# Kernel tuning notes

Hardware: AMD Instinct MI355X
Metric: run time of the kernel (lower is better)

## Reference

```python
import jax, jax.numpy as jnp
import numpy as np

N_NODES = 100000
N_EDGES = 3200000  # avg degree 32
D_IN = 256
D_OUT = 256


def setup_inputs() -> dict:
    key = jax.random.key(0)
    k1, k2, k3, k4 = jax.random.split(key, 4)
    x = jax.random.normal(k1, (N_NODES, D_IN), dtype=jnp.float32)
    # nn.Linear(in, out, bias=False): weight shape [out, in]
    W = jax.random.normal(k2, (D_OUT, D_IN), dtype=jnp.float32) / np.sqrt(D_IN).astype(np.float32)
    bias = jnp.zeros((D_OUT,), dtype=jnp.float32)
    rows = jax.random.randint(k3, (N_EDGES,), 0, N_NODES, dtype=jnp.int32)
    cols = jax.random.randint(k4, (N_EDGES,), 0, N_NODES, dtype=jnp.int32)
    return {"x": x, "W": W, "bias": bias, "rows": rows, "cols": cols}


def reference(x, W, bias, rows, cols):
    # aggr == 'planetoid-gcn-residual' branch; dropout p=0 (identity).
    n = x.shape[0]
    h = x @ W.T + bias                                      # [N, D_out]
    # adj_t.sum(dim=-1): per-row degree of binary adjacency
    deg = jax.ops.segment_sum(jnp.ones(rows.shape, x.dtype), rows, num_segments=n)
    norm = jax.lax.rsqrt(1.0 + deg)[:, None]                # [N, 1]
    h = norm * h
    # spmm_add(adj_t, h)[i] = sum_{(i,j) in E} h[j]
    agg = jax.ops.segment_sum(h[cols], rows, num_segments=n)
    h = agg + h
    return norm * h
```

## Files before the change

kernel.cpp:

```cpp
#include <hip/hip_runtime.h>
#include <hip/hip_fp16.h>
#include <stdint.h>


#define THREADS 256
#define NB 512
#define B3_EDGES 8192

typedef _Float16 half8 __attribute__((ext_vector_type(8)));
typedef float floatx4 __attribute__((ext_vector_type(4)));

__global__ __launch_bounds__(THREADS) void bucket_count(
    const int* __restrict__ rows, int* __restrict__ bcnt, int E, int nbuck) {
    __shared__ int h[NB];
    h[threadIdx.x] = 0; h[threadIdx.x + 256] = 0;
    __syncthreads();
    int nquad  = E >> 2;
    int stride = gridDim.x * THREADS;
    for (int q = blockIdx.x * THREADS + threadIdx.x; q < nquad; q += stride) {
        int4 r = ((const int4*)rows)[q];
        atomicAdd(&h[r.x >> 8], 1);
        atomicAdd(&h[r.y >> 8], 1);
        atomicAdd(&h[r.z >> 8], 1);
        atomicAdd(&h[r.w >> 8], 1);
    }
    if (blockIdx.x == 0)
        for (int e = (nquad << 2) + threadIdx.x; e < E; e += THREADS)
            atomicAdd(&h[rows[e] >> 8], 1);
    __syncthreads();
    for (int b = threadIdx.x; b < nbuck; b += THREADS) {
        int v = h[b];
        if (v) atomicAdd(&bcnt[b], v);
    }
}

__global__ __launch_bounds__(THREADS) void bucket_scan(
    const int* __restrict__ bcnt, int* __restrict__ boff, int* __restrict__ bcur,
    int nbuck, int E) {
    __shared__ int s1[THREADS];
    int tid = threadIdx.x;
    int b0 = 2 * tid, b1 = 2 * tid + 1;
    int v0 = (b0 < nbuck) ? bcnt[b0] : 0;
    int v1 = (b1 < nbuck) ? bcnt[b1] : 0;
    s1[tid] = v0 + v1;
    __syncthreads();
    for (int off = 1; off < THREADS; off <<= 1) {
        int t = (tid >= off) ? s1[tid - off] : 0;
        __syncthreads();
        s1[tid] += t;
        __syncthreads();
    }
    int excl = s1[tid] - (v0 + v1);
    if (b0 < nbuck) { boff[b0] = excl;      bcur[b0] = excl; }
    if (b1 < nbuck) { boff[b1] = excl + v0; bcur[b1] = excl + v0; }
    if (tid == 0) boff[nbuck] = E;
}

__global__ __launch_bounds__(THREADS) void bucket_scatter(
    const int* __restrict__ rows, const int* __restrict__ cols,
    int* __restrict__ bcur, uint32_t* __restrict__ buf, int E, int nbuck) {
    __shared__ uint32_t staged[B3_EDGES];
    __shared__ int h[NB], lo[NB], gb[NB], hc[NB], s1[THREADS];
    int tid = threadIdx.x;
    h[tid] = 0; h[tid + 256] = 0;
    __syncthreads();
    int e0 = blockIdx.x * B3_EDGES;
    int e1 = e0 + B3_EDGES; if (e1 > E) e1 = E;
    for (int e = e0 + tid; e < e1; e += THREADS)
        atomicAdd(&h[rows[e] >> 8], 1);
    __syncthreads();
    int a0 = h[2 * tid], a1 = h[2 * tid + 1];
    s1[tid] = a0 + a1;
    __syncthreads();
    for (int off = 1; off < THREADS; off <<= 1) {
        int t = (tid >= off) ? s1[tid - off] : 0;
        __syncthreads();
        s1[tid] += t;
        __syncthreads();
    }
    int eps = s1[tid] - (a0 + a1);
    lo[2 * tid]     = eps;
    lo[2 * tid + 1] = eps + a0;
    for (int b = tid; b < NB; b += THREADS) {
        int v = h[b];
        gb[b] = (b < nbuck && v) ? atomicAdd(&bcur[b], v) : 0;
        hc[b] = 0;
    }
    __syncthreads();
    for (int e = e0 + tid; e < e1; e += THREADS) {
        int r = rows[e];
        int c = cols[e];
        int b = r >> 8;
        int p = lo[b] + atomicAdd(&hc[b], 1);
        staged[p] = ((uint32_t)(r & 255) << 17) | (uint32_t)c;
    }
    __syncthreads();
    int wid = tid >> 6, lane = tid & 63;
    for (int b = wid; b < nbuck; b += 4) {
        int cnt = h[b], src = lo[b], dst = gb[b];
        for (int i = lane; i < cnt; i += 64)
            buf[dst + i] = staged[src + i];
    }
}

__global__ __launch_bounds__(THREADS) void csr_finalize(
    const uint32_t* __restrict__ buf, const int* __restrict__ boff,
    int* __restrict__ rs, int* __restrict__ csr, int n, int E) {
    int b   = blockIdx.x;
    int tid = threadIdx.x;
    __shared__ int h[256], base[256], s1[THREADS];
    h[tid] = 0;
    __syncthreads();
    int s = boff[b], e = boff[b + 1];
    for (int i = s + tid; i < e; i += THREADS)
        atomicAdd(&h[buf[i] >> 17], 1);
    __syncthreads();
    int v = h[tid];
    s1[tid] = v;
    __syncthreads();
    for (int off = 1; off < THREADS; off <<= 1) {
        int t = (tid >= off) ? s1[tid - off] : 0;
        __syncthreads();
        s1[tid] += t;
        __syncthreads();
    }
    int myBase = s + s1[tid] - v;
    base[tid] = myBase;
    int row = (b << 8) + tid;
    if (row < n) rs[row] = myBase;
    h[tid] = 0;
    if (b == 0 && tid == 0) rs[n] = E;
    __syncthreads();
    for (int i = s + tid; i < e; i += THREADS) {
        uint32_t p = buf[i];
        int rl = p >> 17;
        int c  = p & 0x1FFFF;
        int q  = base[rl] + atomicAdd(&h[rl], 1);
        csr[q] = c;
    }
}

__global__ void make_bswz(const float* __restrict__ W, half8* __restrict__ Bswz) {
    int t = blockIdx.x * THREADS + threadIdx.x;
    int n_tile = t >> 9;
    int k_step = (t >> 6) & 7;
    int lane   = t & 63;
    int q = lane >> 4, m16 = lane & 15;
    const float* src = W + (size_t)(n_tile * 16 + m16) * 256 + k_step * 32 + q * 8;
    half8 h;
#pragma unroll
    for (int j = 0; j < 8; j++) h[j] = (_Float16)src[j];
    Bswz[t] = h;
}

__device__ __forceinline__ int As_swz(int b) {
    return b ^ ((((b >> 10) & 7) ^ (((b >> 8) & 1) << 3)) << 4);
}

__global__ __launch_bounds__(THREADS) void gemm_mfma(
    const float* __restrict__ x, const half8* __restrict__ Bswz,
    const float* __restrict__ bias, const int* __restrict__ rs,
    _Float16* __restrict__ h16, int n) {
    __shared__ _Float16 As[4 * 8 * 64 * 8];
    int tid  = threadIdx.x;
    int row0 = blockIdx.x * 64;

#pragma unroll
    for (int i = 0; i < 16; i++) {
        int flat = i * THREADS + tid;
        int r  = flat >> 6;
        int k  = (flat & 63) * 4;
        float4 v;
        if (row0 + r < n) v = *(const float4*)(x + (size_t)(row0 + r) * 256 + k);
        else { v.x = 0.f; v.y = 0.f; v.z = 0.f; v.w = 0.f; }
        int m_sub  = r >> 4;
        int k_step = k >> 5;
        int q      = (k >> 3) & 3;
        int j      = k & 7;
        int lane_w = (r & 15) + (q << 4);
        int entry  = (m_sub * 8 + k_step) * 64 + lane_w;
        union { _Float16 h[4]; uint2 u; } pk;
        pk.h[0] = (_Float16)v.x; pk.h[1] = (_Float16)v.y;
        pk.h[2] = (_Float16)v.z; pk.h[3] = (_Float16)v.w;
        *(uint2*)((char*)As + As_swz(entry * 16 + (j << 1))) = pk.u;
    }
    __syncthreads();

    int w    = tid >> 6;
    int lane = tid & 63;

    floatx4 acc[4][4];
#pragma unroll
    for (int ms = 0; ms < 4; ms++)
#pragma unroll
        for (int nn = 0; nn < 4; nn++) {
            acc[ms][nn][0] = 0.f; acc[ms][nn][1] = 0.f;
            acc[ms][nn][2] = 0.f; acc[ms][nn][3] = 0.f;
        }

    for (int ks = 0; ks < 8; ks++) {
        half8 bfrag[4];
#pragma unroll
        for (int nn = 0; nn < 4; nn++)
            bfrag[nn] = Bswz[((w * 4 + nn) * 8 + ks) * 64 + lane];
        half8 afrag[4];
#pragma unroll
        for (int ms = 0; ms < 4; ms++)
            afrag[ms] = *(const half8*)((char*)As +
                            As_swz(((ms * 8 + ks) * 64 + lane) * 16));
#pragma unroll
        for (int ms = 0; ms < 4; ms++)
#pragma unroll
            for (int nn = 0; nn < 4; nn++)
                acc[ms][nn] = __builtin_amdgcn_mfma_f32_16x16x32_f16(
                    afrag[ms], bfrag[nn], acc[ms][nn], 0, 0, 0);
    }

    int rgrp = lane >> 4;
    int cl   = lane & 15;
#pragma unroll
    for (int ms = 0; ms < 4; ms++) {
        int rbase = row0 + ms * 16 + rgrp * 4;
        float nrm[4];
#pragma unroll
        for (int i = 0; i < 4; i++) {
            int r = rbase + i;
            nrm[i] = (r < n) ? rsqrtf(1.0f + (float)(rs[r + 1] - rs[r])) : 0.f;
        }
#pragma unroll
        for (int nn = 0; nn < 4; nn++) {
            int col = w * 64 + nn * 16 + cl;
            float bb = bias[col];
#pragma unroll
            for (int i = 0; i < 4; i++) {
                int r = rbase + i;
                if (r < n)
                    h16[(size_t)r * 256 + col] =
                        (_Float16)((acc[ms][nn][i] + bb) * nrm[i]);
            }
        }
    }
}

__global__ __launch_bounds__(THREADS) void agg_rows(
    const _Float16* __restrict__ h16, const int* __restrict__ csr_col,
    const int* __restrict__ rs, float* __restrict__ out, int r0, int r1) {
    int row = r0 + blockIdx.x * 4 + (threadIdx.x >> 6);
    if (row >= r1) return;
    int lane = threadIdx.x & 63;
    int half = lane >> 5;
    int l32  = lane & 31;
    int off  = l32 * 8;

    int s   = rs[row];
    int end = rs[row + 1];

    float acc[8] = {0.f, 0.f, 0.f, 0.f, 0.f, 0.f, 0.f, 0.f};
    if (half == 0) {
        half8 v = *(const half8*)(h16 + (size_t)row * 256 + off);
#pragma unroll
        for (int j = 0; j < 8; j++) acc[j] = (float)v[j];
    }

    int e = s + half;
    for (; e + 2 < end; e += 4) {
        int c0 = csr_col[e];
        int c1 = csr_col[e + 2];
        half8 v0 = *(const half8*)(h16 + (size_t)c0 * 256 + off);
        half8 v1 = *(const half8*)(h16 + (size_t)c1 * 256 + off);
#pragma unroll
        for (int j = 0; j < 8; j++) acc[j] += (float)v0[j] + (float)v1[j];
    }
    for (; e < end; e += 2) {
        int c = csr_col[e];
        half8 v = *(const half8*)(h16 + (size_t)c * 256 + off);
#pragma unroll
        for (int j = 0; j < 8; j++) acc[j] += (float)v[j];
    }

#pragma unroll
    for (int j = 0; j < 8; j++) acc[j] += __shfl_down(acc[j], 32);

    if (half == 0) {
        float nrm = rsqrtf(1.0f + (float)(end - s));
        floatx4 o0, o1;
        o0[0] = acc[0] * nrm; o0[1] = acc[1] * nrm; o0[2] = acc[2] * nrm; o0[3] = acc[3] * nrm;
        o1[0] = acc[4] * nrm; o1[1] = acc[5] * nrm; o1[2] = acc[6] * nrm; o1[3] = acc[7] * nrm;
        float* dst = out + (size_t)row * 256 + off;
        __builtin_nontemporal_store(o0, (floatx4*)dst);
        __builtin_nontemporal_store(o1, (floatx4*)(dst + 4));
    }
}

extern "C" void kernel_launch(void* const* d_in, const int* in_sizes, int n_in,
                              void* d_out, int out_size, void* d_ws, size_t ws_size,
                              hipStream_t stream) {
    const float* x    = (const float*)d_in[0];
    const float* W    = (const float*)d_in[1];
    const float* bias = (const float*)d_in[2];
    const int*   rows = (const int*)d_in[3];
    const int*   cols = (const int*)d_in[4];

    const int D = 256;
    int n = in_sizes[0] / D;
    int E = in_sizes[3];
    int nbuck = (n + 255) >> 8;

    char* p = (char*)d_ws;
    auto alignup = [](size_t v) { return (v + 255) & ~(size_t)255; };
    _Float16* h16 = (_Float16*)p; p += alignup((size_t)n * D * sizeof(_Float16));
    int*   rs     = (int*)p;    p += alignup((size_t)(n + 1) * sizeof(int));
    int*   csr    = (int*)p;    p += alignup((size_t)E * sizeof(int));
    half8* Bswz   = (half8*)p;  p += alignup((size_t)8192 * sizeof(half8));
    int*   bcnt   = (int*)p;    p += alignup((size_t)NB * sizeof(int));
    int*   boff   = (int*)p;    p += alignup((size_t)(NB + 1) * sizeof(int));
    int*   bcur   = (int*)p;    p += alignup((size_t)NB * sizeof(int));

    uint32_t* buf = (uint32_t*)h16;

    hipMemsetAsync(bcnt, 0, (size_t)nbuck * sizeof(int), stream);

    bucket_count<<<256, THREADS, 0, stream>>>(rows, bcnt, E, nbuck);
    bucket_scan<<<1, THREADS, 0, stream>>>(bcnt, boff, bcur, nbuck, E);

    int b3blocks = (E + B3_EDGES - 1) / B3_EDGES;
    bucket_scatter<<<b3blocks, THREADS, 0, stream>>>(rows, cols, bcur, buf, E, nbuck);

    csr_finalize<<<nbuck, THREADS, 0, stream>>>(buf, boff, rs, csr, n, E);

    make_bswz<<<32, THREADS, 0, stream>>>(W, Bswz);

    int gblocks = (n + 63) / 64;
    gemm_mfma<<<gblocks, THREADS, 0, stream>>>(x, Bswz, bias, rs, h16, n);

    int chunk = (n + 7) / 8;
    for (int d = 0; d < 8; ++d) {
        int a0 = d * chunk;
        int a1 = a0 + chunk; if (a1 > n) a1 = n;
        if (a0 >= a1) break;
        int ablocks = (a1 - a0 + 3) / 4;
        agg_rows<<<ablocks, THREADS, 0, stream>>>(h16, csr, rs, (float*)d_out, a0, a1);
    }
}
```

Before: 595.8 us.

## Simplify GEMM A staging, double-buffer MFMA fragments, launch aggregation as two halves

After: 548.2 us. -8.0%, faster.

```diff
diff --git a/kernel.cpp b/kernel.cpp
--- a/kernel.cpp
+++ b/kernel.cpp
@@ -153,10 +153,6 @@
     Bswz[t] = h;
 }
 
-__device__ __forceinline__ int As_swz(int b) {
-    return b ^ ((((b >> 10) & 7) ^ (((b >> 8) & 1) << 3)) << 4);
-}
-
 __global__ __launch_bounds__(THREADS) void gemm_mfma(
     const float* __restrict__ x, const half8* __restrict__ Bswz,
     const float* __restrict__ bias, const int* __restrict__ rs,
@@ -166,23 +162,28 @@
     int row0 = blockIdx.x * 64;
 
 #pragma unroll
-    for (int i = 0; i < 16; i++) {
-        int flat = i * THREADS + tid;
-        int r  = flat >> 6;
-        int k  = (flat & 63) * 4;
-        float4 v;
-        if (row0 + r < n) v = *(const float4*)(x + (size_t)(row0 + r) * 256 + k);
-        else { v.x = 0.f; v.y = 0.f; v.z = 0.f; v.w = 0.f; }
-        int m_sub  = r >> 4;
-        int k_step = k >> 5;
-        int q      = (k >> 3) & 3;
-        int j      = k & 7;
-        int lane_w = (r & 15) + (q << 4);
-        int entry  = (m_sub * 8 + k_step) * 64 + lane_w;
-        union { _Float16 h[4]; uint2 u; } pk;
-        pk.h[0] = (_Float16)v.x; pk.h[1] = (_Float16)v.y;
-        pk.h[2] = (_Float16)v.z; pk.h[3] = (_Float16)v.w;
-        *(uint2*)((char*)As + As_swz(entry * 16 + (j << 1))) = pk.u;
+    for (int i = 0; i < 8; i++) {
+        int entry  = i * 256 + tid;
+        int m_sub  = entry >> 9;
+        int k_step = (entry >> 6) & 7;
+        int lw     = entry & 63;
+        int r      = m_sub * 16 + (lw & 15);
+        int k      = k_step * 32 + (lw >> 4) * 8;
+        float4 v0, v1;
+        if (row0 + r < n) {
+            const float* src = x + (size_t)(row0 + r) * 256 + k;
+            v0 = *(const float4*)src;
+            v1 = *(const float4*)(src + 4);
+        } else {
+            v0.x = v0.y = v0.z = v0.w = 0.f;
+            v1.x = v1.y = v1.z = v1.w = 0.f;
+        }
+        union { _Float16 h[8]; uint4 u; } pk;
+        pk.h[0] = (_Float16)v0.x; pk.h[1] = (_Float16)v0.y;
+        pk.h[2] = (_Float16)v0.z; pk.h[3] = (_Float16)v0.w;
+        pk.h[4] = (_Float16)v1.x; pk.h[5] = (_Float16)v1.y;
+        pk.h[6] = (_Float16)v1.z; pk.h[7] = (_Float16)v1.w;
+        *(uint4*)(As + entry * 8) = pk.u;
     }
     __syncthreads();
 
@@ -198,22 +199,31 @@
             acc[ms][nn][2] = 0.f; acc[ms][nn][3] = 0.f;
         }
 
+    half8 bf[2][4], af[2][4];
+#pragma unroll
+    for (int nn = 0; nn < 4; nn++)
+        bf[0][nn] = Bswz[((w * 4 + nn) * 8 + 0) * 64 + lane];
+#pragma unroll
+    for (int ms = 0; ms < 4; ms++)
+        af[0][ms] = *(const half8*)(As + ((ms * 8 + 0) * 64 + lane) * 8);
+
+#pragma unroll
     for (int ks = 0; ks < 8; ks++) {
-        half8 bfrag[4];
-#pragma unroll
-        for (int nn = 0; nn < 4; nn++)
-            bfrag[nn] = Bswz[((w * 4 + nn) * 8 + ks) * 64 + lane];
-        half8 afrag[4];
-#pragma unroll
-        for (int ms = 0; ms < 4; ms++)
-            afrag[ms] = *(const half8*)((char*)As +
-                            As_swz(((ms * 8 + ks) * 64 + lane) * 16));
+        int cur = ks & 1, nxt = cur ^ 1;
+        if (ks < 7) {
+#pragma unroll
+            for (int nn = 0; nn < 4; nn++)
+                bf[nxt][nn] = Bswz[((w * 4 + nn) * 8 + ks + 1) * 64 + lane];
+#pragma unroll
+            for (int ms = 0; ms < 4; ms++)
+                af[nxt][ms] = *(const half8*)(As + ((ms * 8 + ks + 1) * 64 + lane) * 8);
+        }
 #pragma unroll
         for (int ms = 0; ms < 4; ms++)
 #pragma unroll
             for (int nn = 0; nn < 4; nn++)
                 acc[ms][nn] = __builtin_amdgcn_mfma_f32_16x16x32_f16(
-                    afrag[ms], bfrag[nn], acc[ms][nn], 0, 0, 0);
+                    af[cur][ms], bf[cur][nn], acc[ms][nn], 0, 0, 0);
     }
 
     int rgrp = lane >> 4;
@@ -333,12 +343,9 @@
     int gblocks = (n + 63) / 64;
     gemm_mfma<<<gblocks, THREADS, 0, stream>>>(x, Bswz, bias, rs, h16, n);
 
-    int chunk = (n + 7) / 8;
-    for (int d = 0; d < 8; ++d) {
-        int a0 = d * chunk;
-        int a1 = a0 + chunk; if (a1 > n) a1 = n;
-        if (a0 >= a1) break;
-        int ablocks = (a1 - a0 + 3) / 4;
-        agg_rows<<<ablocks, THREADS, 0, stream>>>(h16, csr, rs, (float*)d_out, a0, a1);
-    }
-}
+    int half_n = (n + 1) / 2;
+    int ab0 = (half_n + 3) / 4;
+    int ab1 = ((n - half_n) + 3) / 4;
+    agg_rows<<<ab0, THREADS, 0, stream>>>(h16, csr, rs, (float*)d_out, 0, half_n);
+    agg_rows<<<ab1, THREADS, 0, stream>>>(h16, csr, rs, (float*)d_out, half_n, n);
+}
```
